# Kernel tuning notes

Measured on AMD Instinct MI355X. Metric: run time of the kernel, lower is better.

## Reference

```python
import jax, jax.numpy as jnp
from jax import lax
import numpy as np

N = 60000   # total nodes
B = 8       # graphs in batch
GS = N // B # nodes per graph
F = 384     # input node features
E = 600000  # edges
H = 6       # hiddenSize (hardcoded in source)
C = 10      # num_classes


def setup_inputs() -> dict:
    key = jax.random.key(0)
    ks = jax.random.split(key, 8)
    x = jax.random.normal(ks[0], (N, F), jnp.float32)
    src = jax.random.randint(ks[1], (E,), 0, N, jnp.int32)
    off = jax.random.randint(ks[2], (E,), 1, GS, jnp.int32)  # 1..GS-1 -> no self loops
    dst = (src // GS) * GS + (src % GS + off) % GS           # same-graph endpoint
    batch = jnp.arange(N, dtype=jnp.int32) // GS
    W1 = jax.random.normal(ks[3], (F, H), jnp.float32) * (1.0 / np.sqrt(F))
    b1 = jnp.zeros((H,), jnp.float32)
    W2 = jax.random.normal(ks[4], (H, C), jnp.float32) * (1.0 / np.sqrt(H))
    b2 = jnp.zeros((C,), jnp.float32)
    Wp1 = jax.random.normal(ks[5], (2 * H,), jnp.float32) * (1.0 / np.sqrt(2 * H))
    bp1 = jnp.zeros((), jnp.float32)
    Wp2 = jax.random.normal(ks[6], (2 * C,), jnp.float32) * (1.0 / np.sqrt(2 * C))
    bp2 = jnp.zeros((), jnp.float32)
    return dict(x=x, src=src, dst=dst, batch=batch, W1=W1, b1=b1, W2=W2, b2=b2,
                Wp1=Wp1, bp1=bp1, Wp2=Wp2, bp2=bp2)


def gcn_conv(x, src, dst, evalid, nvalid, W, b):
    # PyG GCNConv: h = x W; add remaining self-loops (weight 1); deg over dst;
    # norm = dinv[src]*dinv[dst]; aggregate to dst; + bias.
    n = x.shape[0]
    h = x @ W
    ef = evalid.astype(h.dtype)
    is_loop = evalid & (src == dst)
    has_loop = jax.ops.segment_sum(is_loop.astype(jnp.int32), dst, num_segments=n) > 0
    add_loop = (nvalid & ~has_loop).astype(h.dtype)
    deg = jax.ops.segment_sum(ef, dst, num_segments=n) + add_loop
    dinv = jnp.where(deg > 0, lax.rsqrt(jnp.maximum(deg, 1e-12)), 0.0)
    coef = ef * dinv[src] * dinv[dst]
    out = jax.ops.segment_sum(h[src] * coef[:, None], dst, num_segments=n)
    out = out + (add_loop * dinv * dinv)[:, None] * h
    return out + b


def edge_pool(x, src, dst, evalid, nvalid, Wp, bp):
    # PyG EdgePooling: raw = lin([x_src||x_dst]); score = softmax(raw, dst) + 0.5;
    # greedy contraction of edges by descending score; new_x = (sum over cluster) * score.
    n, f = x.shape
    raw = x[src] @ Wp[:f] + x[dst] @ Wp[f:] + bp                      # [E]
    rm = jnp.where(evalid, raw, -jnp.inf)
    m = jax.ops.segment_max(rm, dst, num_segments=n)
    m = jnp.where(jnp.isfinite(m), m, 0.0)
    ex = jnp.where(evalid, jnp.exp(raw - m[dst]), 0.0)
    s = jax.ops.segment_sum(ex, dst, num_segments=n)
    score = jnp.where(evalid, ex / jnp.where(s[dst] > 0, s[dst], 1.0), 0.0) + 0.5

    order = jnp.argsort(jnp.where(evalid, -score, jnp.inf))           # descending, invalid last

    def step(rem, edg):
        s_, d_, v_ = edg
        take = v_ & rem[s_] & rem[d_]
        rem = rem.at[s_].set(rem[s_] & ~take)
        rem = rem.at[d_].set(rem[d_] & ~take)
        return rem, take

    _, chosen_sorted = lax.scan(step, nvalid, (src[order], dst[order], evalid[order]))
    chosen = jnp.zeros_like(evalid).at[order].set(chosen_sorted)

    chf = chosen.astype(x.dtype)
    nonself = src != dst
    dead = jax.ops.segment_sum((chosen & nonself).astype(jnp.int32), dst, num_segments=n) > 0
    new_valid = nvalid & ~dead

    # merged feature: (x_src + x_dst) * score at slot src; unmatched: x * 1
    added = jnp.zeros_like(x).at[src].add((chf * nonself.astype(x.dtype))[:, None] * x[dst])
    scale = 1.0 + jnp.zeros((n,), x.dtype).at[src].add(chf * (score - 1.0))
    new_x = jnp.where(new_valid[:, None], (x + added) * scale[:, None], 0.0)

    # cluster map (dst of chosen edge -> src slot), remap + coalesce (dedup) edges
    merged_src = jnp.full((n,), -1, jnp.int32).at[dst].max(jnp.where(chosen, src, -1))
    cmap = jnp.where(merged_src >= 0, merged_src, jnp.arange(n, dtype=jnp.int32))
    ns, nd = cmap[src], cmap[dst]
    ns_k = jnp.where(evalid, ns, n)  # push invalid edges to the end
    order2 = jnp.lexsort((nd, ns_k))
    ss, dd = ns_k[order2], nd[order2]
    diff = (ss[1:] != ss[:-1]) | (dd[1:] != dd[:-1])
    first = jnp.concatenate([jnp.ones((1,), bool), diff])
    new_evalid = jnp.zeros_like(evalid).at[order2].set(first & evalid[order2])
    return new_x, ns, nd, new_evalid, new_valid


def _forward(x, src, dst, batch, W1, b1, W2, b2, Wp1, bp1, Wp2, bp2):
    evalid = jnp.ones((src.shape[0],), bool)
    nvalid = jnp.ones((x.shape[0],), bool)
    h = jax.nn.relu(gcn_conv(x, src, dst, evalid, nvalid, W1, b1))
    # dropout: identity in eval mode
    h, s1, d1, ev1, nv1 = edge_pool(h, src, dst, evalid, nvalid, Wp1, bp1)
    h = gcn_conv(h, s1, d1, ev1, nv1, W2, b2)
    h, s2, d2, ev2, nv2 = edge_pool(h, s1, d1, ev1, nv1, Wp2, bp2)
    nvf = nv2.astype(h.dtype)
    cnt = jax.ops.segment_sum(nvf, batch, num_segments=B)
    sm = jax.ops.segment_sum(h * nvf[:, None], batch, num_segments=B)
    g = sm / cnt[:, None]
    return jax.nn.log_softmax(g, axis=1)


def reference(x, src, dst, batch, W1, b1, W2, b2, Wp1, bp1, Wp2, bp2):
    return _forward(x, src, dst, batch, W1, b1, W2, b2, Wp1, bp1, Wp2, bp2)
```

## Files before the change

kernel.cpp:

```cpp
#include <hip/hip_runtime.h>
#include <math.h>

#define NN 60000
#define BB 8
#define GS 7500
#define FF 384
#define EE 600000
#define HH 6
#define CC 10
#define HT_BITS 20
#define HT_SIZE (1u << HT_BITS)
#define HT_MASK (HT_SIZE - 1u)
#define TPB 256
#define CAP 80000
#define REMW ((GS + 31) / 32)
#define GPAD 32
#define SCAN_B 1024
#define NBLK ((NN + SCAN_B - 1) / SCAN_B)
static_assert(NBLK <= 64, "scan3 wave-scan assumes <=64 blocks");
static_assert((HH % 2) == 0 && (CC % 2) == 0, "float2 paths assume even fd");

static inline int ngrid(int n) { return (n + TPB - 1) / TPB; }

__device__ __forceinline__ unsigned long long mkprio(float sc, int e) {
  return (((unsigned long long)__float_as_uint(sc)) << 32) |
         (unsigned int)(~(unsigned int)e);
}

__global__ void k_mm1(const float* __restrict__ x, const float* __restrict__ W,
                      float* __restrict__ out) {
  __shared__ float Ws[FF * HH];
  for (int i = threadIdx.x; i < FF * HH; i += blockDim.x) Ws[i] = W[i];
  __syncthreads();
  int wave = threadIdx.x >> 6, lane = threadIdx.x & 63;
  int node = blockIdx.x * 4 + wave;
  if (node >= NN) return;
  const float* xr = x + (size_t)node * FF;
  float acc[HH] = {0.f, 0.f, 0.f, 0.f, 0.f, 0.f};
  for (int k = lane; k < FF; k += 64) {
    float xv = xr[k];
#pragma unroll
    for (int j = 0; j < HH; j++) acc[j] += xv * Ws[k * HH + j];
  }
#pragma unroll
  for (int j = 0; j < HH; j++) {
#pragma unroll
    for (int o = 32; o > 0; o >>= 1) acc[j] += __shfl_down(acc[j], o, 64);
  }
  if (lane == 0) {
#pragma unroll
    for (int j = 0; j < HH; j++) out[(size_t)node * HH + j] = acc[j];
  }
}

__global__ void k_prep(float* __restrict__ deg, unsigned char* __restrict__ hasloop,
                       int* __restrict__ gcntsA,
                       int* __restrict__ gcntsB, float* __restrict__ gsum,
                       float* __restrict__ gcnt, const unsigned char* __restrict__ nvin,
                       unsigned char* __restrict__ nvout, float* __restrict__ scale,
                       int* __restrict__ merged, int* __restrict__ partner,
                       unsigned long long* __restrict__ bestA,
                       unsigned long long* __restrict__ bestB,
                       unsigned char* __restrict__ remG) {
  int v = blockIdx.x * blockDim.x + threadIdx.x;
  if (v >= NN) return;
  deg[v] = 0.f;
  hasloop[v] = 0;
  unsigned char nvv = nvin ? nvin[v] : 1;
  nvout[v] = nvv;
  remG[v] = nvv;
  bestA[v] = 0ULL;
  bestB[v] = 0ULL;
  scale[v] = 1.0f;
  if (merged) merged[v] = -1;
  partner[v] = -1;
  if (v < BB * GPAD) { gcntsA[v] = 0; gcntsB[v] = 0; }
  if (v < BB * CC) gsum[v] = 0.f;
  if (v < BB) gcnt[v] = 0.f;
}

__global__ void k_deg(const int* __restrict__ src, const int* __restrict__ dst,
                      const unsigned char* __restrict__ ev, float* __restrict__ deg,
                      unsigned char* __restrict__ hasloop) {
  int e = blockIdx.x * blockDim.x + threadIdx.x;
  if (e >= EE) return;
  if (ev && !ev[e]) return;
  int d = dst[e];
  atomicAdd(&deg[d], 1.0f);
  if (src[e] == d) hasloop[d] = 1;
}

__global__ __launch_bounds__(1024) void k_scan1(const float* __restrict__ deg,
                                                int* __restrict__ rowstart,
                                                int* __restrict__ bsum) {
  __shared__ int tmp[SCAN_B];
  int t = threadIdx.x;
  int i = blockIdx.x * SCAN_B + t;
  int v = (i < NN) ? (int)deg[i] : 0;
  tmp[t] = v;
  __syncthreads();
  for (int o = 1; o < SCAN_B; o <<= 1) {
    int y = (t >= o) ? tmp[t - o] : 0;
    __syncthreads();
    tmp[t] += y;
    __syncthreads();
  }
  if (i < NN) rowstart[i] = tmp[t] - v;
  if (t == SCAN_B - 1) bsum[blockIdx.x] = tmp[t];
}

__global__ void k_scan3(int* __restrict__ rowstart, const int* __restrict__ bsum,
                        int* __restrict__ fill, const float* __restrict__ deg,
                        const unsigned char* __restrict__ hasloop,
                        const unsigned char* __restrict__ nv, float* __restrict__ dinv,
                        unsigned char* __restrict__ addloop) {
  __shared__ int offs[64];
  __shared__ int total;
  int t = threadIdx.x;
  if (t < 64) {
    int v = (t < NBLK) ? bsum[t] : 0;
    int x = v;
#pragma unroll
    for (int o = 1; o < 64; o <<= 1) {
      int y = __shfl_up(x, o, 64);
      if (t >= o) x += y;
    }
    offs[t] = x - v;
    if (t == 63) total = x;
  }
  __syncthreads();
  int i = blockIdx.x * blockDim.x + t;
  if (i >= NN) return;
  int r = rowstart[i] + offs[i >> 10];
  rowstart[i] = r;
  fill[i] = r;
  if (i == NN - 1) rowstart[NN] = total;
  int nvv = nv ? (int)nv[i] : 1;
  unsigned char al = (nvv && !hasloop[i]) ? 1 : 0;
  float d = deg[i] + (float)al;
  dinv[i] = d > 0.f ? 1.0f / sqrtf(fmaxf(d, 1e-12f)) : 0.f;
  addloop[i] = al;
}

__global__ void k_scatter(const int* __restrict__ src, const int* __restrict__ dst,
                          const unsigned char* __restrict__ ev, int* __restrict__ fill,
                          int* __restrict__ csrS, int* __restrict__ csrE) {
  int e = blockIdx.x * blockDim.x + threadIdx.x;
  if (e >= EE) return;
  if (ev && !ev[e]) return;
  int d = dst[e];
  int p = atomicAdd(&fill[d], 1);
  csrS[p] = src[e];
  csrE[p] = e;
}

template <int FD>
__global__ void k_agg_fin(const int* __restrict__ rowstart, const int* __restrict__ csrS,
                          const float* __restrict__ dinv, const unsigned char* __restrict__ addloop,
                          const float* __restrict__ h, const float* __restrict__ b,
                          float* __restrict__ out, int relu) {
  int v = blockIdx.x * blockDim.x + threadIdx.x;
  if (v >= NN) return;
  int b0 = rowstart[v], b1 = rowstart[v + 1];
  float acc[FD];
#pragma unroll
  for (int j = 0; j < FD; j++) acc[j] = 0.f;
  float dv = dinv[v];
  for (int i = b0; i < b1; i++) {
    int s = csrS[i];
    float c = dinv[s] * dv;
    const float2* hr2 = (const float2*)(h + (size_t)s * FD);
#pragma unroll
    for (int j = 0; j < FD / 2; j++) {
      float2 hv = hr2[j];
      acc[2 * j] += hv.x * c;
      acc[2 * j + 1] += hv.y * c;
    }
  }
  float cl = addloop[v] ? dv * dv : 0.f;
  const float* hv = h + (size_t)v * FD;
#pragma unroll
  for (int j = 0; j < FD; j++) {
    float o = acc[j] + cl * hv[j] + b[j];
    if (relu) o = fmaxf(o, 0.f);
    out[(size_t)v * FD + j] = o;
  }
}

__global__ void k_raw(const float* __restrict__ x, const int* __restrict__ src,
                      const int* __restrict__ dst, const unsigned char* __restrict__ ev,
                      const float* __restrict__ Wp, const float* __restrict__ bp,
                      float* __restrict__ raw, unsigned char* __restrict__ chosen, int fd) {
  int e = blockIdx.x * blockDim.x + threadIdx.x;
  if (e >= EE) return;
  chosen[e] = 0;
  if (ev && !ev[e]) return;
  int s = src[e], d = dst[e];
  float r = bp[0];
  const float2* xs = (const float2*)(x + (size_t)s * fd);
  const float2* xd = (const float2*)(x + (size_t)d * fd);
  int h2 = fd >> 1;
  for (int j = 0; j < h2; j++) {
    float2 v = xs[j];
    r += v.x * Wp[2 * j];
    r += v.y * Wp[2 * j + 1];
  }
  for (int j = 0; j < h2; j++) {
    float2 v = xd[j];
    r += v.x * Wp[fd + 2 * j];
    r += v.y * Wp[fd + 2 * j + 1];
  }
  raw[e] = r;
}

__global__ void k_smscore(const int* __restrict__ rowstart, const int* __restrict__ csrS,
                          const int* __restrict__ csrE, const float* __restrict__ raw,
                          const unsigned char* __restrict__ remG, float* __restrict__ score,
                          unsigned long long* __restrict__ bestA) {
  int v = blockIdx.x * blockDim.x + threadIdx.x;
  if (v >= NN) return;
  int b0 = rowstart[v], b1 = rowstart[v + 1];
  if (b0 == b1) return;
  float m = -INFINITY;
  for (int i = b0; i < b1; i++) m = fmaxf(m, raw[csrE[i]]);
  float s = 0.f;
  for (int i = b0; i < b1; i++) s += expf(raw[csrE[i]] - m);
  if (!remG[v]) return;
  float sd = s > 0.f ? s : 1.0f;
  unsigned long long lb = 0ULL;
  for (int i = b0; i < b1; i++) {
    int sv = csrS[i];
    if (!remG[sv]) continue;
    int e = csrE[i];
    float sc = expf(raw[e] - m) / sd + 0.5f;
    score[e] = sc;
    unsigned long long p = mkprio(sc, e);
    if (p > lb) lb = p;
    if (sv != v && p > bestA[sv]) atomicMax(&bestA[sv], p);
  }
  if (lb > bestA[v]) atomicMax(&bestA[v], lb);
}

__global__ void k_r1sel(const int* __restrict__ src, const int* __restrict__ dst,
                        const float* __restrict__ score, const unsigned char* __restrict__ ev,
                        unsigned char* __restrict__ remG,
                        const unsigned long long* __restrict__ bestA,
                        unsigned long long* __restrict__ bestB,
                        unsigned char* __restrict__ chosen, ulonglong2* __restrict__ recs,
                        int* __restrict__ gcnts) {
  __shared__ int wcnt[TPB / 64][BB];
  __shared__ int bbase[BB];
  int e = blockIdx.x * blockDim.x + threadIdx.x;
  int w = threadIdx.x >> 6, lane = threadIdx.x & 63;
  int keep = 0, s = 0, d = 0, g = 0;
  unsigned long long p = 0;
  if (e < EE && (!ev || ev[e])) {
    s = src[e];
    d = dst[e];
    g = s / GS;
    if (remG[s] && remG[d]) {
      p = mkprio(score[e], e);
      if (bestA[s] == p && bestA[d] == p) {
        chosen[e] = 1;
        remG[s] = 0;
        remG[d] = 0;
      } else {
        keep = 1;
        bestB[s] = 0ULL;
        bestB[d] = 0ULL;
      }
    }
  }
  int myrank = 0;
#pragma unroll
  for (int gg = 0; gg < BB; gg++) {
    unsigned long long m = __ballot(keep && g == gg);
    if (keep && g == gg) myrank = __popcll(m & ((1ULL << lane) - 1ULL));
    if (lane == 0) wcnt[w][gg] = __popcll(m);
  }
  __syncthreads();
  if (threadIdx.x < BB) {
    int gg = threadIdx.x, tot = 0;
#pragma unroll
    for (int ww = 0; ww < TPB / 64; ww++) {
      int c = wcnt[ww][gg];
      wcnt[ww][gg] = tot;
      tot += c;
    }
    bbase[gg] = tot ? atomicAdd(&gcnts[gg * GPAD], tot) : 0;
  }
  __syncthreads();
  if (keep)
    recs[(size_t)g * CAP + bbase[g] + wcnt[w][g] + myrank] =
        make_ulonglong2(p, (((unsigned long long)(unsigned int)s) << 32) | (unsigned int)d);
}

__global__ void k_gpost(const ulonglong2* __restrict__ recs, const int* __restrict__ gcnts,
                        const unsigned char* __restrict__ remG,
                        unsigned long long* __restrict__ bestC, int* __restrict__ gcntsOut) {
  int g = blockIdx.y;
  if (blockIdx.x == 0 && threadIdx.x == 0) gcntsOut[g * GPAD] = 0;
  int n = gcnts[g * GPAD];
  const ulonglong2* lst = recs + (size_t)g * CAP;
  int stride = gridDim.x * blockDim.x;
  for (int i = blockIdx.x * blockDim.x + threadIdx.x; i < n; i += stride) {
    ulonglong2 r = lst[i];
    int s = (int)(r.y >> 32), d = (int)(r.y & 0xFFFFFFFFu);
    if (remG[s] && remG[d]) {
      if (r.x > bestC[s]) atomicMax(&bestC[s], r.x);
      if (d != s && r.x > bestC[d]) atomicMax(&bestC[d], r.x);
    }
  }
}

__global__ void k_gsel(const ulonglong2* __restrict__ recsIn, const int* __restrict__ gcntsIn,
                       unsigned char* __restrict__ remG,
                       const unsigned long long* __restrict__ bestC,
                       unsigned long long* __restrict__ bestN,
                       unsigned char* __restrict__ chosen, ulonglong2* __restrict__ recsOut,
                       int* __restrict__ gcntsOut) {
  int g = blockIdx.y;
  int n = gcntsIn[g * GPAD];
  const ulonglong2* lst = recsIn + (size_t)g * CAP;
  ulonglong2* outl = recsOut + (size_t)g * CAP;
  int lane = threadIdx.x & 63;
  int stride = gridDim.x * blockDim.x;
  for (int i = blockIdx.x * blockDim.x + threadIdx.x; i - lane < n; i += stride) {
    int keep = 0;
    ulonglong2 r;
    if (i < n) {
      r = lst[i];
      int s = (int)(r.y >> 32), d = (int)(r.y & 0xFFFFFFFFu);
      if (remG[s] && remG[d]) {
        if (bestC[s] == r.x && bestC[d] == r.x) {
          int e = (int)(~(unsigned int)(r.x & 0xFFFFFFFFu));
          chosen[e] = 1;
          remG[s] = 0;
          remG[d] = 0;
        } else {
          keep = 1;
          bestN[s] = 0ULL;
          bestN[d] = 0ULL;
        }
      }
    }
    unsigned long long m = __ballot(keep);
    int tot = __popcll(m);
    int pre = __popcll(m & ((1ULL << lane) - 1ULL));
    int b0 = 0;
    if (lane == 0 && tot) b0 = atomicAdd(&gcntsOut[g * GPAD], tot);
    b0 = __shfl(b0, 0, 64);
    if (keep) outl[b0 + pre] = r;
  }
}

__global__ __launch_bounds__(1024) void k_match_g(ulonglong2* __restrict__ recs0,
                                                  ulonglong2* __restrict__ recs1,
                                                  const int* __restrict__ gcnts,
                                                  const unsigned char* __restrict__ remG,
                                                  unsigned char* __restrict__ chosen) {
  __shared__ unsigned long long best[GS];
  __shared__ unsigned int remB[REMW];
  __shared__ int cnt_next;
  const int g = blockIdx.x;
  const int base = g * GS;
  const int t = threadIdx.x, nth = blockDim.x;
  const int lane = t & 63;

  for (int w = t; w < REMW; w += nth) {
    unsigned int bits = 0;
    int v0 = w * 32;
    if (v0 + 32 <= GS) {
      const unsigned int* p4 = (const unsigned int*)(remG + base + v0);
#pragma unroll
      for (int q = 0; q < 8; q++) {
        unsigned int x4 = p4[q];
        bits |= ((x4 & 1u) << (q * 4)) | (((x4 >> 8) & 1u) << (q * 4 + 1)) |
                (((x4 >> 16) & 1u) << (q * 4 + 2)) | (((x4 >> 24) & 1u) << (q * 4 + 3));
      }
    } else {
      for (int b = 0; b < 32; b++) {
        int v = v0 + b;
        if (v < GS) bits |= (remG[base + v] ? 1u : 0u) << b;
      }
    }
    remB[w] = bits;
  }
  for (int i = t; i < GS; i += nth) best[i] = 0ULL;
  __syncthreads();

  ulonglong2* bufs[2] = {recs0 + (size_t)g * CAP, recs1 + (size_t)g * CAP};
  int n = gcnts[g * GPAD];
  int cur = 0;
  int guard = 0;

  while (n > 0) {
    if (++guard > 100000) break;
    for (int i0 = 0; i0 < n; i0 += nth * 4) {
      ulonglong2 r[4];
      int have[4];
#pragma unroll
      for (int k = 0; k < 4; k++) {
        int i = i0 + t + k * nth;
        have[k] = i < n;
        if (have[k]) r[k] = bufs[cur][i];
      }
#pragma unroll
      for (int k = 0; k < 4; k++) {
        if (!have[k]) continue;
        int ls = (int)(r[k].y >> 32) - base, ld = (int)(r[k].y & 0xFFFFFFFFu) - base;
        if (((remB[ls >> 5] >> (ls & 31)) & 1u) && ((remB[ld >> 5] >> (ld & 31)) & 1u)) {
          atomicMax(&best[ls], r[k].x);
          if (ld != ls) atomicMax(&best[ld], r[k].x);
        }
      }
    }
    if (t == 0) cnt_next = 0;
    __syncthreads();
    for (int i0 = 0; i0 < n; i0 += nth * 4) {
      ulonglong2 r[4];
      int have[4];
#pragma unroll
      for (int k = 0; k < 4; k++) {
        int i = i0 + t + k * nth;
        have[k] = i < n;
        if (have[k]) r[k] = bufs[cur][i];
      }
#pragma unroll
      for (int k = 0; k < 4; k++) {
        int keep = 0;
        int ls = 0, ld = 0;
        if (have[k]) {
          ls = (int)(r[k].y >> 32) - base;
          ld = (int)(r[k].y & 0xFFFFFFFFu) - base;
          if (((remB[ls >> 5] >> (ls & 31)) & 1u) && ((remB[ld >> 5] >> (ld & 31)) & 1u)) {
            if (best[ls] == r[k].x && best[ld] == r[k].x) {
              int e = (int)(~(unsigned int)(r[k].x & 0xFFFFFFFFu));
              chosen[e] = 1;
              atomicAnd(&remB[ls >> 5], ~(1u << (ls & 31)));
              atomicAnd(&remB[ld >> 5], ~(1u << (ld & 31)));
            } else {
              keep = 1;
            }
          }
        }
        unsigned long long m = __ballot(keep);
        int tot = __popcll(m);
        int pre = __popcll(m & ((1ULL << lane) - 1ULL));
        int b0 = 0;
        if (lane == 0 && tot) b0 = atomicAdd(&cnt_next, tot);
        b0 = __shfl(b0, 0, 64);
        if (keep) bufs[cur ^ 1][b0 + pre] = r[k];
      }
    }
    __syncthreads();
    n = cnt_next;
    if (n < 4096) {
      for (int i = t; i < n; i += nth) {
        ulonglong2 r = bufs[cur ^ 1][i];
        best[(int)(r.y >> 32) - base] = 0ULL;
        best[(int)(r.y & 0xFFFFFFFFu) - base] = 0ULL;
      }
    } else {
      for (int i = t; i < GS; i += nth) best[i] = 0ULL;
    }
    __syncthreads();
    cur ^= 1;
  }
}

__global__ void k_pool_edge(const int* __restrict__ src, const int* __restrict__ dst,
                            const unsigned char* __restrict__ chosen, const float* __restrict__ score,
                            unsigned char* __restrict__ nvout, float* __restrict__ scale,
                            int* __restrict__ partner, int* __restrict__ merged) {
  int e = blockIdx.x * blockDim.x + threadIdx.x;
  if (e >= EE) return;
  if (!chosen[e]) return;
  int s = src[e], d = dst[e];
  scale[s] = score[e];
  if (merged) merged[d] = s;
  if (s != d) {
    nvout[d] = 0;
    partner[s] = d;
  }
}

__global__ void k_newx_mm2(const float* __restrict__ h1, const int* __restrict__ partner,
                           const float* __restrict__ scale, const unsigned char* __restrict__ nvout,
                           const float* __restrict__ W2, float* __restrict__ h2pre) {
  int v = blockIdx.x * blockDim.x + threadIdx.x;
  if (v >= NN) return;
  float sc = scale[v];
  int ok = nvout[v];
  int p = partner[v];
  float nx[HH];
#pragma unroll
  for (int j = 0; j < HH; j++) {
    float a = h1[(size_t)v * HH + j];
    if (p >= 0) a += h1[(size_t)p * HH + j];
    nx[j] = ok ? a * sc : 0.f;
  }
#pragma unroll
  for (int c = 0; c < CC; c++) {
    float a = 0.f;
#pragma unroll
    for (int j = 0; j < HH; j++) a += nx[j] * W2[j * CC + c];
    h2pre[(size_t)v * CC + c] = a;
  }
}

__device__ __forceinline__ unsigned int ht_hash(unsigned long long key) {
  return (unsigned int)((key * 0x9E3779B97F4A7C15ULL) >> 44) & HT_MASK;
}

__global__ void k_remap_ins(const int* __restrict__ src, const int* __restrict__ dst,
                            const int* __restrict__ merged, int* __restrict__ ns,
                            int* __restrict__ nd, unsigned long long* __restrict__ htab) {
  int e = blockIdx.x * blockDim.x + threadIdx.x;
  if (e >= EE) return;
  int s = src[e], d = dst[e];
  int ms = merged[s], md = merged[d];
  int a = ms >= 0 ? ms : s;
  int b = md >= 0 ? md : d;
  ns[e] = a;
  nd[e] = b;
  unsigned long long key =
      (unsigned long long)((((unsigned int)a) << 16) | (unsigned int)b);
  unsigned long long val = (key << 32) | (unsigned int)e;
  unsigned int h = ht_hash(key);
  for (;;) {
    unsigned long long curv = htab[h];
    if (curv == ~0ULL) {
      unsigned long long prev = atomicCAS(&htab[h], ~0ULL, val);
      if (prev == ~0ULL) break;
      curv = prev;
    }
    if ((curv >> 32) == key) {
      if ((curv & 0xFFFFFFFFULL) > (unsigned long long)(unsigned int)e)
        atomicMin(&htab[h], val);
      break;
    }
    h = (h + 1) & HT_MASK;
  }
}

__global__ void k_dedup_deg(const int* __restrict__ ns, const int* __restrict__ nd,
                            const unsigned long long* __restrict__ htab,
                            unsigned char* __restrict__ evout, float* __restrict__ deg,
                            unsigned char* __restrict__ hasloop) {
  int e = blockIdx.x * blockDim.x + threadIdx.x;
  if (e >= EE) return;
  unsigned long long key =
      (unsigned long long)((((unsigned int)ns[e]) << 16) | (unsigned int)nd[e]);
  unsigned int h = ht_hash(key);
  for (;;) {
    unsigned long long curv = htab[h];
    if ((curv >> 32) == key) {
      unsigned char ev = ((curv & 0xFFFFFFFFULL) == (unsigned long long)(unsigned int)e) ? 1 : 0;
      evout[e] = ev;
      if (ev) {
        int d = nd[e];
        atomicAdd(&deg[d], 1.0f);
        if (ns[e] == d) hasloop[d] = 1;
      }
      return;
    }
    h = (h + 1) & HT_MASK;
  }
}

__global__ void k_newx_pool(const float* __restrict__ h2, const int* __restrict__ partner,
                            const float* __restrict__ scale, const unsigned char* __restrict__ nv,
                            float* __restrict__ gsum, float* __restrict__ gcnt) {
  int v = blockIdx.x * blockDim.x + threadIdx.x;
  int lane = threadIdx.x & 63;
  int b = (v < NN ? v : NN - 1) / GS;
  int active = (v < NN) && nv[v];
  float cnt = active ? 1.f : 0.f;
  float val[CC];
  if (active) {
    float sc = scale[v];
    int p = partner[v];
    for (int j = 0; j < CC; j++) {
      float a = h2[(size_t)v * CC + j];
      if (p >= 0) a += h2[(size_t)p * CC + j];
      val[j] = a * sc;
    }
  } else {
    for (int j = 0; j < CC; j++) val[j] = 0.f;
  }
  int b0 = __shfl(b, 0, 64);
  unsigned long long same = __ballot(b == b0);
  if (same == ~0ULL) {
    for (int o = 32; o > 0; o >>= 1) {
      cnt += __shfl_down(cnt, o, 64);
      for (int j = 0; j < CC; j++) val[j] += __shfl_down(val[j], o, 64);
    }
    if (lane == 0 && cnt > 0.f) {
      atomicAdd(&gcnt[b0], cnt);
      for (int j = 0; j < CC; j++) atomicAdd(&gsum[b0 * CC + j], val[j]);
    }
  } else if (active) {
    atomicAdd(&gcnt[b], cnt);
    for (int j = 0; j < CC; j++) atomicAdd(&gsum[b * CC + j], val[j]);
  }
}

__global__ void k_logsm(const float* __restrict__ gsum, const float* __restrict__ gcnt,
                        float* __restrict__ out) {
  int t = threadIdx.x;
  if (t >= BB) return;
  float gr[CC];
  float c = gcnt[t];
  float m = -INFINITY;
  for (int j = 0; j < CC; j++) {
    gr[j] = gsum[t * CC + j] / c;
    m = fmaxf(m, gr[j]);
  }
  float s = 0.f;
  for (int j = 0; j < CC; j++) s += expf(gr[j] - m);
  float l = logf(s);
  for (int j = 0; j < CC; j++) out[t * CC + j] = gr[j] - m - l;
}

extern "C" void kernel_launch(void* const* d_in, const int* in_sizes, int n_in,
                              void* d_out, int out_size, void* d_ws, size_t ws_size,
                              hipStream_t stream) {
  const float* x = (const float*)d_in[0];
  const int* src = (const int*)d_in[1];
  const int* dst = (const int*)d_in[2];
  const float* W1 = (const float*)d_in[4];
  const float* b1 = (const float*)d_in[5];
  const float* W2 = (const float*)d_in[6];
  const float* b2 = (const float*)d_in[7];
  const float* Wp1 = (const float*)d_in[8];
  const float* bp1 = (const float*)d_in[9];
  const float* Wp2 = (const float*)d_in[10];
  const float* bp2 = (const float*)d_in[11];
  float* out = (float*)d_out;

  char* wsb = (char*)d_ws;
  size_t off = 0;
  auto A = [&](size_t bytes) -> char* {
    char* r = wsb + off;
    off = (off + bytes + 255) & ~(size_t)255;
    return r;
  };
  float* h1pre = (float*)A((size_t)NN * HH * 4);
  float* h1out = (float*)A((size_t)NN * HH * 4);
  float* deg = (float*)A((size_t)NN * 4);
  float* dinv = (float*)A((size_t)NN * 4);
  unsigned char* hasloop = (unsigned char*)A(NN);
  unsigned char* addloop = (unsigned char*)A(NN);
  float* raw = (float*)A((size_t)EE * 4);
  float* score = (float*)A((size_t)EE * 4);
  unsigned char* chosen = (unsigned char*)A(EE);
  unsigned char* nv1 = (unsigned char*)A(NN);
  unsigned char* nv2 = (unsigned char*)A(NN);
  float* scale = (float*)A((size_t)NN * 4);
  int* partner = (int*)A((size_t)NN * 4);
  int* merged = (int*)A((size_t)NN * 4);
  int* ns = (int*)A((size_t)EE * 4);
  int* nd = (int*)A((size_t)EE * 4);
  unsigned char* ev1 = (unsigned char*)A(EE);
  unsigned long long* htab = (unsigned long long*)A((size_t)HT_SIZE * 8);
  float* h2pre = (float*)A((size_t)NN * CC * 4);
  float* h2out = (float*)A((size_t)NN * CC * 4);
  unsigned long long* bestA = (unsigned long long*)A((size_t)NN * 8);
  unsigned long long* bestB = (unsigned long long*)A((size_t)NN * 8);
  unsigned char* remG = (unsigned char*)A(NN);
  ulonglong2* recs0 = (ulonglong2*)A((size_t)BB * CAP * 16);
  ulonglong2* recs1 = (ulonglong2*)A((size_t)BB * CAP * 16);
  int* gcntsA = (int*)A((size_t)BB * GPAD * 4);
  int* gcntsB = (int*)A((size_t)BB * GPAD * 4);
  float* gsum = (float*)A((size_t)BB * CC * 4);
  float* gcnt = (float*)A((size_t)BB * 4);
  int* rowstart = (int*)A((size_t)(NN + 1) * 4);
  int* fill = (int*)A((size_t)NN * 4);
  int* bsum = (int*)A((size_t)64 * 4);
  int* csrS = (int*)A((size_t)EE * 4);
  int* csrE = (int*)A((size_t)EE * 4);
  (void)ws_size; (void)n_in; (void)in_sizes; (void)out_size;

  const int GE = ngrid(EE), GN = ngrid(NN);
  const dim3 RG(32, BB);

  hipMemsetAsync(htab, 0xFF, (size_t)HT_SIZE * 8, stream);
  hipLaunchKernelGGL(k_mm1, dim3((NN + 3) / 4), dim3(TPB), 0, stream, x, W1, h1pre);
  hipLaunchKernelGGL(k_prep, dim3(GN), dim3(TPB), 0, stream, deg, hasloop, gcntsA, gcntsB,
                     gsum, gcnt, (const unsigned char*)nullptr, nv1, scale, merged, partner, bestA, bestB, remG);
  hipLaunchKernelGGL(k_deg, dim3(GE), dim3(TPB), 0, stream, src, dst, (const unsigned char*)nullptr, deg, hasloop);
  hipLaunchKernelGGL(k_scan1, dim3(NBLK), dim3(SCAN_B), 0, stream, deg, rowstart, bsum);
  hipLaunchKernelGGL(k_scan3, dim3(GN), dim3(TPB), 0, stream, rowstart, bsum, fill, deg, hasloop,
                     (const unsigned char*)nullptr, dinv, addloop);
  hipLaunchKernelGGL(k_scatter, dim3(GE), dim3(TPB), 0, stream, src, dst, (const unsigned char*)nullptr, fill, csrS, csrE);
  hipLaunchKernelGGL(k_agg_fin<HH>, dim3(GN), dim3(TPB), 0, stream, rowstart, csrS, dinv, addloop, h1pre, b1, h1out, 1);

  hipLaunchKernelGGL(k_raw, dim3(GE), dim3(TPB), 0, stream, h1out, src, dst, (const unsigned char*)nullptr, Wp1, bp1, raw, chosen, HH);
  hipLaunchKernelGGL(k_smscore, dim3(GN), dim3(TPB), 0, stream, rowstart, csrS, csrE, raw, remG, score, bestA);
  hipLaunchKernelGGL(k_r1sel, dim3(GE), dim3(TPB), 0, stream, src, dst, score, (const unsigned char*)nullptr, remG, bestA, bestB, chosen, recs0, gcntsA);
  hipLaunchKernelGGL(k_gpost, RG, dim3(TPB), 0, stream, recs0, gcntsA, remG, bestB, gcntsB);
  hipLaunchKernelGGL(k_gsel, RG, dim3(TPB), 0, stream, recs0, gcntsA, remG, bestB, bestA, chosen, recs1, gcntsB);
  hipLaunchKernelGGL(k_gpost, RG, dim3(TPB), 0, stream, recs1, gcntsB, remG, bestA, gcntsA);
  hipLaunchKernelGGL(k_gsel, RG, dim3(TPB), 0, stream, recs1, gcntsB, remG, bestA, bestB, chosen, recs0, gcntsA);
  hipLaunchKernelGGL(k_gpost, RG, dim3(TPB), 0, stream, recs0, gcntsA, remG, bestB, gcntsB);
  hipLaunchKernelGGL(k_gsel, RG, dim3(TPB), 0, stream, recs0, gcntsA, remG, bestB, bestA, chosen, recs1, gcntsB);
  hipLaunchKernelGGL(k_gpost, RG, dim3(TPB), 0, stream, recs1, gcntsB, remG, bestA, gcntsA);
  hipLaunchKernelGGL(k_gsel, RG, dim3(TPB), 0, stream, recs1, gcntsB, remG, bestA, bestB, chosen, recs0, gcntsA);
  hipLaunchKernelGGL(k_gpost, RG, dim3(TPB), 0, stream, recs0, gcntsA, remG, bestB, gcntsB);
  hipLaunchKernelGGL(k_gsel, RG, dim3(TPB), 0, stream, recs0, gcntsA, remG, bestB, bestA, chosen, recs1, gcntsB);
  hipLaunchKernelGGL(k_match_g, dim3(BB), dim3(1024), 0, stream, recs1, recs0, gcntsB, remG, chosen);
  hipLaunchKernelGGL(k_pool_edge, dim3(GE), dim3(TPB), 0, stream, src, dst, chosen, score, nv1, scale, partner, merged);
  hipLaunchKernelGGL(k_newx_mm2, dim3(GN), dim3(TPB), 0, stream, h1out, partner, scale, nv1, W2, h2pre);
  hipLaunchKernelGGL(k_remap_ins, dim3(GE), dim3(TPB), 0, stream, src, dst, merged, ns, nd, htab);

  hipLaunchKernelGGL(k_prep, dim3(GN), dim3(TPB), 0, stream, deg, hasloop, gcntsA, gcntsB,
                     gsum, gcnt, (const unsigned char*)nv1, nv2, scale, (int*)nullptr, partner, bestA, bestB, remG);
  hipLaunchKernelGGL(k_dedup_deg, dim3(GE), dim3(TPB), 0, stream, ns, nd, htab, ev1, deg, hasloop);
  hipLaunchKernelGGL(k_scan1, dim3(NBLK), dim3(SCAN_B), 0, stream, deg, rowstart, bsum);
  hipLaunchKernelGGL(k_scan3, dim3(GN), dim3(TPB), 0, stream, rowstart, bsum, fill, deg, hasloop,
                     (const unsigned char*)nv1, dinv, addloop);
  hipLaunchKernelGGL(k_scatter, dim3(GE), dim3(TPB), 0, stream, ns, nd, (const unsigned char*)ev1, fill, csrS, csrE);
  hipLaunchKernelGGL(k_agg_fin<CC>, dim3(GN), dim3(TPB), 0, stream, rowstart, csrS, dinv, addloop, h2pre, b2, h2out, 0);

  hipLaunchKernelGGL(k_raw, dim3(GE), dim3(TPB), 0, stream, h2out, ns, nd, (const unsigned char*)ev1, Wp2, bp2, raw, chosen, CC);
  hipLaunchKernelGGL(k_smscore, dim3(GN), dim3(TPB), 0, stream, rowstart, csrS, csrE, raw, remG, score, bestA);
  hipLaunchKernelGGL(k_r1sel, dim3(GE), dim3(TPB), 0, stream, ns, nd, score, (const unsigned char*)ev1, remG, bestA, bestB, chosen, recs0, gcntsA);
  hipLaunchKernelGGL(k_gpost, RG, dim3(TPB), 0, stream, recs0, gcntsA, remG, bestB, gcntsB);
  hipLaunchKernelGGL(k_gsel, RG, dim3(TPB), 0, stream, recs0, gcntsA, remG, bestB, bestA, chosen, recs1, gcntsB);
  hipLaunchKernelGGL(k_gpost, RG, dim3(TPB), 0, stream, recs1, gcntsB, remG, bestA, gcntsA);
  hipLaunchKernelGGL(k_gsel, RG, dim3(TPB), 0, stream, recs1, gcntsB, remG, bestA, bestB, chosen, recs0, gcntsA);
  hipLaunchKernelGGL(k_gpost, RG, dim3(TPB), 0, stream, recs0, gcntsA, remG, bestB, gcntsB);
  hipLaunchKernelGGL(k_gsel, RG, dim3(TPB), 0, stream, recs0, gcntsA, remG, bestB, bestA, chosen, recs1, gcntsB);
  hipLaunchKernelGGL(k_gpost, RG, dim3(TPB), 0, stream, recs1, gcntsB, remG, bestA, gcntsA);
  hipLaunchKernelGGL(k_gsel, RG, dim3(TPB), 0, stream, recs1, gcntsB, remG, bestA, bestB, chosen, recs0, gcntsA);
  hipLaunchKernelGGL(k_gpost, RG, dim3(TPB), 0, stream, recs0, gcntsA, remG, bestB, gcntsB);
  hipLaunchKernelGGL(k_gsel, RG, dim3(TPB), 0, stream, recs0, gcntsA, remG, bestB, bestA, chosen, recs1, gcntsB);
  hipLaunchKernelGGL(k_match_g, dim3(BB), dim3(1024), 0, stream, recs1, recs0, gcntsB, remG, chosen);
  hipLaunchKernelGGL(k_pool_edge, dim3(GE), dim3(TPB), 0, stream, ns, nd, chosen, score, nv2, scale, partner, (int*)nullptr);

  hipLaunchKernelGGL(k_newx_pool, dim3(GN), dim3(TPB), 0, stream, h2out, partner, scale, nv2, gsum, gcnt);
  hipLaunchKernelGGL(k_logsm, dim3(1), dim3(64), 0, stream, gsum, gcnt, out);
}
```

Before: 1.405 ms.

## Drop per-edge raw kernel via softmax shift invariance; fuse prep into newx

After: 1.330 ms. 1.06x faster.

```diff
diff --git a/kernel.cpp b/kernel.cpp
--- a/kernel.cpp
+++ b/kernel.cpp
@@ -158,6 +158,7 @@
 __global__ void k_agg_fin(const int* __restrict__ rowstart, const int* __restrict__ csrS,
                           const float* __restrict__ dinv, const unsigned char* __restrict__ addloop,
                           const float* __restrict__ h, const float* __restrict__ b,
+                          const float* __restrict__ Wp, float* __restrict__ aout,
                           float* __restrict__ out, int relu) {
   int v = blockIdx.x * blockDim.x + threadIdx.x;
   if (v >= NN) return;
@@ -179,52 +180,29 @@
   }
   float cl = addloop[v] ? dv * dv : 0.f;
   const float* hv = h + (size_t)v * FD;
+  float av = 0.f;
 #pragma unroll
   for (int j = 0; j < FD; j++) {
     float o = acc[j] + cl * hv[j] + b[j];
     if (relu) o = fmaxf(o, 0.f);
     out[(size_t)v * FD + j] = o;
-  }
-}
-
-__global__ void k_raw(const float* __restrict__ x, const int* __restrict__ src,
-                      const int* __restrict__ dst, const unsigned char* __restrict__ ev,
-                      const float* __restrict__ Wp, const float* __restrict__ bp,
-                      float* __restrict__ raw, unsigned char* __restrict__ chosen, int fd) {
-  int e = blockIdx.x * blockDim.x + threadIdx.x;
-  if (e >= EE) return;
-  chosen[e] = 0;
-  if (ev && !ev[e]) return;
-  int s = src[e], d = dst[e];
-  float r = bp[0];
-  const float2* xs = (const float2*)(x + (size_t)s * fd);
-  const float2* xd = (const float2*)(x + (size_t)d * fd);
-  int h2 = fd >> 1;
-  for (int j = 0; j < h2; j++) {
-    float2 v = xs[j];
-    r += v.x * Wp[2 * j];
-    r += v.y * Wp[2 * j + 1];
-  }
-  for (int j = 0; j < h2; j++) {
-    float2 v = xd[j];
-    r += v.x * Wp[fd + 2 * j];
-    r += v.y * Wp[fd + 2 * j + 1];
-  }
-  raw[e] = r;
+    av += o * Wp[j];
+  }
+  aout[v] = av;
 }
 
 __global__ void k_smscore(const int* __restrict__ rowstart, const int* __restrict__ csrS,
-                          const int* __restrict__ csrE, const float* __restrict__ raw,
+                          const int* __restrict__ csrE, const float* __restrict__ a,
                           const unsigned char* __restrict__ remG, float* __restrict__ score,
                           unsigned long long* __restrict__ bestA) {
   int v = blockIdx.x * blockDim.x + threadIdx.x;
   if (v >= NN) return;
   int b0 = rowstart[v], b1 = rowstart[v + 1];
   if (b0 == b1) return;
-  float m = -INFINITY;
-  for (int i = b0; i < b1; i++) m = fmaxf(m, raw[csrE[i]]);
+  float ma = -INFINITY;
+  for (int i = b0; i < b1; i++) ma = fmaxf(ma, a[csrS[i]]);
   float s = 0.f;
-  for (int i = b0; i < b1; i++) s += expf(raw[csrE[i]] - m);
+  for (int i = b0; i < b1; i++) s += expf(a[csrS[i]] - ma);
   if (!remG[v]) return;
   float sd = s > 0.f ? s : 1.0f;
   unsigned long long lb = 0ULL;
@@ -232,7 +210,7 @@
     int sv = csrS[i];
     if (!remG[sv]) continue;
     int e = csrE[i];
-    float sc = expf(raw[e] - m) / sd + 0.5f;
+    float sc = expf(a[sv] - ma) / sd + 0.5f;
     score[e] = sc;
     unsigned long long p = mkprio(sc, e);
     if (p > lb) lb = p;
@@ -254,6 +232,7 @@
   int w = threadIdx.x >> 6, lane = threadIdx.x & 63;
   int keep = 0, s = 0, d = 0, g = 0;
   unsigned long long p = 0;
+  if (e < EE) chosen[e] = 0;
   if (e < EE && (!ev || ev[e])) {
     s = src[e];
     d = dst[e];
@@ -485,13 +464,22 @@
   }
 }
 
-__global__ void k_newx_mm2(const float* __restrict__ h1, const int* __restrict__ partner,
-                           const float* __restrict__ scale, const unsigned char* __restrict__ nvout,
-                           const float* __restrict__ W2, float* __restrict__ h2pre) {
+__global__ void k_newx_prep(const float* __restrict__ h1, const float* __restrict__ W2,
+                            float* __restrict__ h2pre,
+                            float* __restrict__ deg, unsigned char* __restrict__ hasloop,
+                            int* __restrict__ gcntsA, int* __restrict__ gcntsB,
+                            float* __restrict__ gsum, float* __restrict__ gcnt,
+                            const unsigned char* __restrict__ nv1,
+                            unsigned char* __restrict__ nv2, float* __restrict__ scale,
+                            int* __restrict__ partner,
+                            unsigned long long* __restrict__ bestA,
+                            unsigned long long* __restrict__ bestB,
+                            unsigned char* __restrict__ remG) {
   int v = blockIdx.x * blockDim.x + threadIdx.x;
   if (v >= NN) return;
   float sc = scale[v];
-  int ok = nvout[v];
+  unsigned char nvv = nv1[v];
+  int ok = nvv;
   int p = partner[v];
   float nx[HH];
 #pragma unroll
@@ -507,6 +495,17 @@
     for (int j = 0; j < HH; j++) a += nx[j] * W2[j * CC + c];
     h2pre[(size_t)v * CC + c] = a;
   }
+  deg[v] = 0.f;
+  hasloop[v] = 0;
+  nv2[v] = nvv;
+  remG[v] = nvv;
+  bestA[v] = 0ULL;
+  bestB[v] = 0ULL;
+  scale[v] = 1.0f;
+  partner[v] = -1;
+  if (v < BB * GPAD) { gcntsA[v] = 0; gcntsB[v] = 0; }
+  if (v < BB * CC) gsum[v] = 0.f;
+  if (v < BB) gcnt[v] = 0.f;
 }
 
 __device__ __forceinline__ unsigned int ht_hash(unsigned long long key) {
@@ -638,6 +637,7 @@
   const float* Wp2 = (const float*)d_in[10];
   const float* bp2 = (const float*)d_in[11];
   float* out = (float*)d_out;
+  (void)bp1; (void)bp2;
 
   char* wsb = (char*)d_ws;
   size_t off = 0;
@@ -652,7 +652,7 @@
   float* dinv = (float*)A((size_t)NN * 4);
   unsigned char* hasloop = (unsigned char*)A(NN);
   unsigned char* addloop = (unsigned char*)A(NN);
-  float* raw = (float*)A((size_t)EE * 4);
+  float* aout = (float*)A((size_t)NN * 4);
   float* score = (float*)A((size_t)EE * 4);
   unsigned char* chosen = (unsigned char*)A(EE);
   unsigned char* nv1 = (unsigned char*)A(NN);
@@ -694,10 +694,9 @@
   hipLaunchKernelGGL(k_scan3, dim3(GN), dim3(TPB), 0, stream, rowstart, bsum, fill, deg, hasloop,
                      (const unsigned char*)nullptr, dinv, addloop);
   hipLaunchKernelGGL(k_scatter, dim3(GE), dim3(TPB), 0, stream, src, dst, (const unsigned char*)nullptr, fill, csrS, csrE);
-  hipLaunchKernelGGL(k_agg_fin<HH>, dim3(GN), dim3(TPB), 0, stream, rowstart, csrS, dinv, addloop, h1pre, b1, h1out, 1);
-
-  hipLaunchKernelGGL(k_raw, dim3(GE), dim3(TPB), 0, stream, h1out, src, dst, (const unsigned char*)nullptr, Wp1, bp1, raw, chosen, HH);
-  hipLaunchKernelGGL(k_smscore, dim3(GN), dim3(TPB), 0, stream, rowstart, csrS, csrE, raw, remG, score, bestA);
+  hipLaunchKernelGGL(k_agg_fin<HH>, dim3(GN), dim3(TPB), 0, stream, rowstart, csrS, dinv, addloop, h1pre, b1, Wp1, aout, h1out, 1);
+
+  hipLaunchKernelGGL(k_smscore, dim3(GN), dim3(TPB), 0, stream, rowstart, csrS, csrE, aout, remG, score, bestA);
   hipLaunchKernelGGL(k_r1sel, dim3(GE), dim3(TPB), 0, stream, src, dst, score, (const unsigned char*)nullptr, remG, bestA, bestB, chosen, recs0, gcntsA);
   hipLaunchKernelGGL(k_gpost, RG, dim3(TPB), 0, stream, recs0, gcntsA, remG, bestB, gcntsB);
   hipLaunchKernelGGL(k_gsel, RG, dim3(TPB), 0, stream, recs0, gcntsA, remG, bestB, bestA, chosen, recs1, gcntsB);
@@ -711,20 +710,18 @@
   hipLaunchKernelGGL(k_gsel, RG, dim3(TPB), 0, stream, recs0, gcntsA, remG, bestB, bestA, chosen, recs1, gcntsB);
   hipLaunchKernelGGL(k_match_g, dim3(BB), dim3(1024), 0, stream, recs1, recs0, gcntsB, remG, chosen);
   hipLaunchKernelGGL(k_pool_edge, dim3(GE), dim3(TPB), 0, stream, src, dst, chosen, score, nv1, scale, partner, merged);
-  hipLaunchKernelGGL(k_newx_mm2, dim3(GN), dim3(TPB), 0, stream, h1out, partner, scale, nv1, W2, h2pre);
+  hipLaunchKernelGGL(k_newx_prep, dim3(GN), dim3(TPB), 0, stream, h1out, W2, h2pre,
+                     deg, hasloop, gcntsA, gcntsB, gsum, gcnt, nv1, nv2, scale, partner, bestA, bestB, remG);
   hipLaunchKernelGGL(k_remap_ins, dim3(GE), dim3(TPB), 0, stream, src, dst, merged, ns, nd, htab);
 
-  hipLaunchKernelGGL(k_prep, dim3(GN), dim3(TPB), 0, stream, deg, hasloop, gcntsA, gcntsB,
-                     gsum, gcnt, (const unsigned char*)nv1, nv2, scale, (int*)nullptr, partner, bestA, bestB, remG);
   hipLaunchKernelGGL(k_dedup_deg, dim3(GE), dim3(TPB), 0, stream, ns, nd, htab, ev1, deg, hasloop);
   hipLaunchKernelGGL(k_scan1, dim3(NBLK), dim3(SCAN_B), 0, stream, deg, rowstart, bsum);
   hipLaunchKernelGGL(k_scan3, dim3(GN), dim3(TPB), 0, stream, rowstart, bsum, fill, deg, hasloop,
                      (const unsigned char*)nv1, dinv, addloop);
   hipLaunchKernelGGL(k_scatter, dim3(GE), dim3(TPB), 0, stream, ns, nd, (const unsigned char*)ev1, fill, csrS, csrE);
-  hipLaunchKernelGGL(k_agg_fin<CC>, dim3(GN), dim3(TPB), 0, stream, rowstart, csrS, dinv, addloop, h2pre, b2, h2out, 0);
-
-  hipLaunchKernelGGL(k_raw, dim3(GE), dim3(TPB), 0, stream, h2out, ns, nd, (const unsigned char*)ev1, Wp2, bp2, raw, chosen, CC);
-  hipLaunchKernelGGL(k_smscore, dim3(GN), dim3(TPB), 0, stream, rowstart, csrS, csrE, raw, remG, score, bestA);
+  hipLaunchKernelGGL(k_agg_fin<CC>, dim3(GN), dim3(TPB), 0, stream, rowstart, csrS, dinv, addloop, h2pre, b2, Wp2, aout, h2out, 0);
+
+  hipLaunchKernelGGL(k_smscore, dim3(GN), dim3(TPB), 0, stream, rowstart, csrS, csrE, aout, remG, score, bestA);
   hipLaunchKernelGGL(k_r1sel, dim3(GE), dim3(TPB), 0, stream, ns, nd, score, (const unsigned char*)ev1, remG, bestA, bestB, chosen, recs0, gcntsA);
   hipLaunchKernelGGL(k_gpost, RG, dim3(TPB), 0, stream, recs0, gcntsA, remG, bestB, gcntsB);
   hipLaunchKernelGGL(k_gsel, RG, dim3(TPB), 0, stream, recs0, gcntsA, remG, bestB, bestA, chosen, recs1, gcntsB);
```
